# Kernel optimization log

Hardware: AMD Instinct MI355X
Metric: run time of the kernel (lower is better)

Reference implementation:

```python
import jax, jax.numpy as jnp
import numpy as np

DIM = 768
NUM_HEADS = 12
HEAD_DIM = DIM // NUM_HEADS
SCALE = HEAD_DIM ** (-0.5)
LN_EPS = 1e-5


def setup_inputs() -> dict:
    key = jax.random.key(0)
    ks = jax.random.split(key, 8)
    B, K, C = 4, 2048, DIM
    return {
        "x": jax.random.normal(ks[0], (B, K, C), jnp.float32),
        "pos_embed": jax.random.normal(ks[1], (B, K, C), jnp.float32),
        "rel_pos_bias": jax.random.normal(ks[2], (B, K, K), jnp.float32),
        "ln_g": jnp.ones((C,), jnp.float32),
        "ln_b": jnp.zeros((C,), jnp.float32),
        "qkv_w": jax.random.normal(ks[3], (C, 3 * C), jnp.float32) * 0.02,
        "qkv_b": jnp.zeros((3 * C,), jnp.float32),
        "proj_w": jax.random.normal(ks[4], (C, C), jnp.float32) * 0.02,
        "proj_b": jnp.zeros((C,), jnp.float32),
    }


def _layernorm(x, g, b):
    mu = jnp.mean(x, axis=-1, keepdims=True)
    var = jnp.mean(jnp.square(x - mu), axis=-1, keepdims=True)
    return (x - mu) * jax.lax.rsqrt(var + LN_EPS) * g + b


def reference(x, pos_embed, rel_pos_bias, ln_g, ln_b, qkv_w, qkv_b, proj_w, proj_b):
    B, K, C = x.shape
    H, D = NUM_HEADS, HEAD_DIM
    xp = _layernorm(x, ln_g, ln_b) + pos_embed
    qkv = xp @ qkv_w + qkv_b                      # [B,K,3C]
    qkv = qkv.reshape(B, K, 3, H, D)
    q = jnp.transpose(qkv[:, :, 0], (0, 2, 1, 3))  # [B,H,K,D]
    k = jnp.transpose(qkv[:, :, 1], (0, 2, 1, 3))
    v = jnp.transpose(qkv[:, :, 2], (0, 2, 1, 3))
    attn = jnp.einsum("bhqd,bhkd->bhqk", q, k) * SCALE
    attn = attn + rel_pos_bias[:, None, :, :]
    attn = jax.nn.softmax(attn, axis=-1)
    out = jnp.einsum("bhqk,bhkd->bhqd", attn, v)   # [B,H,K,D]
    out = jnp.transpose(out, (0, 2, 1, 3)).reshape(B, K, C)
    # DropPath(0.1) is identity in eval mode
    return out @ proj_w + proj_b
```

## Files before the change

kernel.cpp:

```cpp
#include <hip/hip_runtime.h>
#include <hip/hip_bf16.h>
#include <stdint.h>

typedef __attribute__((ext_vector_type(4))) float f32x4;
typedef __attribute__((ext_vector_type(16))) float f32x16;
typedef __attribute__((ext_vector_type(8))) short s16x8;
typedef __attribute__((ext_vector_type(4))) short s16x4;
typedef uint16_t u16;

#define DEV __device__ __forceinline__

static DEV u16 f2bf(float f) {
  union { float f; uint32_t u; } v; v.f = f;
  uint32_t r = v.u + 0x7fffu + ((v.u >> 16) & 1u);
  return (u16)(r >> 16);
}

static DEV float bf2f(u16 x) {
  union { uint32_t u; float f; } v; v.u = ((uint32_t)x) << 16;
  return v.f;
}

static DEV uint32_t cvt_pk_bf16(float lo, float hi) {
  uint32_t r;
  asm("v_cvt_pk_bf16_f32 %0, %1, %2" : "=v"(r) : "v"(lo), "v"(hi));
  return r;
}

#if defined(__has_builtin) && __has_builtin(__builtin_amdgcn_exp2f)
static DEV float exp2_fast(float x) { return __builtin_amdgcn_exp2f(x); }
#else
static DEV float exp2_fast(float x) {
  float r;
  asm("v_exp_f32 %0, %1\n\ts_nop 1" : "=v"(r) : "v"(x));
  return r;
}
#endif

#define GLD_LDS16(gp, lp) __builtin_amdgcn_global_load_lds( \
    (const __attribute__((address_space(1))) void*)(gp),    \
    (__attribute__((address_space(3))) void*)(lp), 16, 0, 0)

__global__ __launch_bounds__(256) void k_ln(
    const float* __restrict__ x, const float* __restrict__ pos,
    const float* __restrict__ g, const float* __restrict__ be,
    u16* __restrict__ xp) {
  int row = blockIdx.x;
  size_t base = (size_t)row * 768;
  int t = threadIdx.x;
  float v0 = x[base + t], v1 = x[base + t + 256], v2 = x[base + t + 512];
  float s = v0 + v1 + v2;
  float ss = v0 * v0 + v1 * v1 + v2 * v2;
#pragma unroll
  for (int off = 1; off < 64; off <<= 1) {
    s += __shfl_xor(s, off);
    ss += __shfl_xor(ss, off);
  }
  __shared__ float red[8];
  int wave = t >> 6, lane = t & 63;
  if (lane == 0) { red[wave] = s; red[4 + wave] = ss; }
  __syncthreads();
  float tot = red[0] + red[1] + red[2] + red[3];
  float tss = red[4] + red[5] + red[6] + red[7];
  float mu = tot * (1.0f / 768.0f);
  float var = tss * (1.0f / 768.0f) - mu * mu;
  float rs = rsqrtf(var + 1e-5f);
  float vv[3] = {v0, v1, v2};
#pragma unroll
  for (int i = 0; i < 3; ++i) {
    int c = t + i * 256;
    float val = (vv[i] - mu) * rs * g[c] + be[c] + pos[base + c];
    xp[base + c] = f2bf(val);
  }
}

__global__ __launch_bounds__(256) void k_tr(
    const float* __restrict__ in, u16* __restrict__ out, int K, int N) {
  __shared__ float tile[32][33];
  int n0 = blockIdx.x * 32, k0 = blockIdx.y * 32;
  int tx = threadIdx.x & 31, ty = threadIdx.x >> 5;
#pragma unroll
  for (int r = ty; r < 32; r += 8)
    tile[r][tx] = in[(size_t)(k0 + r) * N + n0 + tx];
  __syncthreads();
#pragma unroll
  for (int r = ty; r < 32; r += 8)
    out[(size_t)(n0 + r) * K + k0 + tx] = f2bf(tile[tx][r]);
}

__global__ __launch_bounds__(256) void k_gemm_qkv(
    const u16* __restrict__ A, const u16* __restrict__ Bt,
    const float* __restrict__ bias, u16* __restrict__ qkv,
    u16* __restrict__ vtg, const float* __restrict__ biasf,
    u16* __restrict__ biasb) {
  __shared__ u16 Al[128 * 64];
  __shared__ u16 Bl[128 * 64];
  const size_t BHKD = (size_t)48 * 2048 * 64;
  int mt = blockIdx.x, nt = blockIdx.y;
  int t = threadIdx.x, wave = t >> 6, lane = t & 63;
  int lr = lane & 15, lg = lane >> 4;
  {
    size_t tid = ((size_t)(nt * 64 + mt) * 256 + t) * 8;
    size_t stride = (size_t)1152 * 256 * 8;
    const size_t NB = (size_t)4 * 2048 * 2048;
    for (size_t i = tid; i < NB; i += stride) {
      f32x4 a = *(const f32x4*)(biasf + i);
      f32x4 b = *(const f32x4*)(biasf + i + 4);
      s16x8 o;
#pragma unroll
      for (int j = 0; j < 4; ++j) o[j] = (short)f2bf(a[j] * 1.4426950409f);
#pragma unroll
      for (int j = 0; j < 4; ++j) o[4 + j] = (short)f2bf(b[j] * 1.4426950409f);
      *(s16x8*)(biasb + i) = o;
    }
  }
  f32x4 acc[4][4];
#pragma unroll
  for (int i = 0; i < 4; ++i)
#pragma unroll
    for (int j = 0; j < 4; ++j) acc[i][j] = (f32x4){0.f, 0.f, 0.f, 0.f};
  const size_t Ab = (size_t)mt * 128 * 768;
  const size_t Bb = (size_t)nt * 128 * 768;
  int wr = (wave >> 1) * 64, wc = (wave & 1) * 64;
  for (int kt = 0; kt < 12; ++kt) {
#pragma unroll
    for (int c = 0; c < 4; ++c) {
      int q = c * 256 + t;
      int row = q >> 3, ch = q & 7;
      int sc = ch ^ (row & 7);
      GLD_LDS16(A + Ab + (size_t)row * 768 + kt * 64 + sc * 8,
                &Al[(size_t)(c * 256 + wave * 64) * 8]);
      GLD_LDS16(Bt + Bb + (size_t)row * 768 + kt * 64 + sc * 8,
                &Bl[(size_t)(c * 256 + wave * 64) * 8]);
    }
    __syncthreads();
#pragma unroll
    for (int ki = 0; ki < 2; ++ki) {
      s16x8 af[4], bf[4];
#pragma unroll
      for (int mi = 0; mi < 4; ++mi)
        af[mi] = *(const s16x8*)&Al[(wr + mi * 16 + lr) * 64 +
                                    (((ki * 4 + lg) ^ (lr & 7)) * 8)];
#pragma unroll
      for (int ni = 0; ni < 4; ++ni)
        bf[ni] = *(const s16x8*)&Bl[(wc + ni * 16 + lr) * 64 +
                                    (((ki * 4 + lg) ^ (lr & 7)) * 8)];
#pragma unroll
      for (int mi = 0; mi < 4; ++mi)
#pragma unroll
        for (int ni = 0; ni < 4; ++ni)
          acc[mi][ni] = __builtin_amdgcn_mfma_f32_16x16x32_bf16(
              af[mi], bf[ni], acc[mi][ni], 0, 0, 0);
    }
    __syncthreads();
  }
  int which0 = (nt * 128) / 768;
  float qscale = (which0 == 0) ? 0.1803368801f : 1.0f;
#pragma unroll
  for (int ni = 0; ni < 4; ++ni) {
    int col = wc + ni * 16 + lr;
    int n = nt * 128 + col;
    int which = n / 768, cc = n % 768;
    int h = cc >> 6, d = cc & 63;
    float bs = bias[n];
    if (which == 2) {
#pragma unroll
      for (int mi = 0; mi < 4; ++mi) {
        int m0 = mt * 128 + wr + mi * 16 + lg * 4;
        int b = m0 >> 11, kp0 = m0 & 2047;
        s16x4 o4;
#pragma unroll
        for (int j = 0; j < 4; ++j) o4[j] = (short)f2bf(acc[mi][ni][j] + bs);
        *(s16x4*)&vtg[((size_t)(b * 12 + h) * 64 + d) * 2048 + kp0] = o4;
      }
    } else {
#pragma unroll
      for (int mi = 0; mi < 4; ++mi) {
#pragma unroll
        for (int j = 0; j < 4; ++j) {
          int row = wr + mi * 16 + lg * 4 + j;
          int m = mt * 128 + row;
          int b = m >> 11, kp = m & 2047;
          size_t dst = (size_t)which * BHKD +
                       (((size_t)b * 12 + h) * 2048 + kp) * 64 + d;
          qkv[dst] = f2bf((acc[mi][ni][j] + bs) * qscale);
        }
      }
    }
  }
}

#define STAGE_KV(KB, VB, ktt) do {                                          \
  _Pragma("unroll")                                                         \
  for (int c_ = 0; c_ < 2; ++c_) {                                          \
    int q_ = c_ * 256 + t; int r_ = q_ >> 3, ch_ = q_ & 7;                  \
    int sc_ = ch_ ^ (r_ & 7);                                               \
    int gk_ = (r_ & 0x33) | ((r_ & 4) << 1) | ((r_ & 8) >> 1);              \
    GLD_LDS16(Kg + ((size_t)((ktt) * 64 + gk_)) * 64 + sc_ * 8,             \
              &KB[(c_ * 256 + wave * 64) * 8]);                             \
    GLD_LDS16(Vt + (size_t)r_ * 2048 + (ktt) * 64 + sc_ * 8,                \
              &VB[(c_ * 256 + wave * 64) * 8]);                             \
  }                                                                         \
} while (0)

#define LOAD_B(BR, ktt) do {                                                \
  const u16* bp_ = Bgl + (ktt) * 64;                                        \
  BR[0] = *(const s16x8*)(bp_);                                             \
  BR[1] = *(const s16x8*)(bp_ + 16);                                        \
  BR[2] = *(const s16x8*)(bp_ + 32);                                        \
  BR[3] = *(const s16x8*)(bp_ + 48);                                        \
} while (0)

#define COMPUTE_TILE(KB, VB, BV) do {                                       \
  f32x16 sa_[2];                                                            \
  _Pragma("unroll")                                                         \
  for (int kv_ = 0; kv_ < 2; ++kv_)                                         \
    _Pragma("unroll")                                                       \
    for (int r = 0; r < 16; ++r)                                            \
      sa_[kv_][r] = bf2f((u16)BV[kv_ * 2 + (r >> 3)][r & 7]);               \
  __builtin_amdgcn_s_setprio(1);                                            \
  _Pragma("unroll")                                                         \
  for (int ki = 0; ki < 4; ++ki) {                                          \
    _Pragma("unroll")                                                       \
    for (int kv_ = 0; kv_ < 2; ++kv_) {                                     \
      s16x8 kf = *(const s16x8*)&KB[(kv_ * 32 + l31) * 64 +                 \
                                    (((ki * 2 + hi) ^ (l31 & 7)) * 8)];     \
      sa_[kv_] = __builtin_amdgcn_mfma_f32_32x32x16_bf16(kf, qf[ki],        \
                                                         sa_[kv_], 0, 0, 0);\
    }                                                                       \
  }                                                                         \
  __builtin_amdgcn_s_setprio(0);                                            \
  float p_[32];                                                             \
  _Pragma("unroll")                                                         \
  for (int kv_ = 0; kv_ < 2; ++kv_)                                         \
    _Pragma("unroll")                                                       \
    for (int r = 0; r < 16; ++r)                                            \
      p_[kv_ * 16 + r] = exp2_fast(sa_[kv_][r]);                            \
  float tm_[16];                                                            \
  _Pragma("unroll")                                                         \
  for (int i = 0; i < 16; ++i) tm_[i] = p_[i] + p_[i + 16];                 \
  _Pragma("unroll")                                                         \
  for (int off = 8; off >= 1; off >>= 1)                                    \
    _Pragma("unroll")                                                       \
    for (int i = 0; i < off; ++i) tm_[i] += tm_[i + off];                   \
  l_run += tm_[0];                                                          \
  union { uint32_t u[4]; s16x8 v; } pa_[4];                                 \
  _Pragma("unroll")                                                         \
  for (int s = 0; s < 4; ++s)                                               \
    _Pragma("unroll")                                                       \
    for (int w = 0; w < 4; ++w)                                             \
      pa_[s].u[w] = cvt_pk_bf16(p_[(s >> 1) * 16 + (s & 1) * 8 + 2 * w],    \
                                p_[(s >> 1) * 16 + (s & 1) * 8 + 2 * w + 1]);\
  __builtin_amdgcn_s_setprio(1);                                            \
  _Pragma("unroll")                                                         \
  for (int s = 0; s < 4; ++s) {                                             \
    _Pragma("unroll")                                                       \
    for (int dt = 0; dt < 2; ++dt) {                                        \
      s16x8 vf = *(const s16x8*)&VB[(dt * 32 + l31) * 64 +                  \
                                    (((s * 2 + hi) ^ (l31 & 7)) * 8)];      \
      oacc[dt] = __builtin_amdgcn_mfma_f32_32x32x16_bf16(vf, pa_[s].v,      \
                                                         oacc[dt], 0, 0, 0);\
    }                                                                       \
  }                                                                         \
  __builtin_amdgcn_s_setprio(0);                                            \
} while (0)

__global__ __launch_bounds__(256, 2) void k_attn(
    const u16* __restrict__ qkv, const u16* __restrict__ vtg,
    const u16* __restrict__ biasb, u16* __restrict__ ctx) {
  __shared__ u16 Kl[3][64 * 64];
  __shared__ u16 Vl[3][64 * 64];
  int bid = blockIdx.x;
  int swz = (bid & 7) * 96 + (bid >> 3);
  int h = swz % 12;
  int bq = swz / 12;
  int qt = bq & 15;
  int b = bq >> 4;
  int bh = b * 12 + h;
  int t = threadIdx.x, wave = t >> 6, lane = t & 63;
  int l31 = lane & 31, hi = lane >> 5;
  const size_t BHKD = (size_t)48 * 2048 * 64;
  const u16* Q = qkv + (size_t)bh * 2048 * 64;
  const u16* Kg = Q + BHKD;
  const u16* Vt = vtg + (size_t)bh * 64 * 2048;
  int qrow = qt * 128 + wave * 32 + l31;
  const u16* Bgl = biasb + ((size_t)b * 2048 + qrow) * 2048 + hi * 8;
  s16x8 qf[4];
#pragma unroll
  for (int ki = 0; ki < 4; ++ki)
    qf[ki] = *(const s16x8*)&Q[(size_t)qrow * 64 + ki * 16 + hi * 8];
  f32x16 oacc[2];
#pragma unroll
  for (int r = 0; r < 16; ++r) { oacc[0][r] = 0.f; oacc[1][r] = 0.f; }
  float l_run = 0.f;

  STAGE_KV(Kl[0], Vl[0], 0);
  STAGE_KV(Kl[1], Vl[1], 1);
  asm volatile("s_waitcnt vmcnt(4)" ::: "memory");
  __builtin_amdgcn_s_barrier();
  __builtin_amdgcn_sched_barrier(0);

  int cur = 0;
#pragma unroll 1
  for (int kt = 0; kt < 32; ++kt) {
    s16x8 bv_[4];
    LOAD_B(bv_, kt);
    int nb = cur + 2; if (nb >= 3) nb -= 3;
    if (kt + 2 < 32) STAGE_KV(Kl[nb], Vl[nb], kt + 2);
    COMPUTE_TILE(Kl[cur], Vl[cur], bv_);
    asm volatile("s_waitcnt vmcnt(4)" ::: "memory");
    __builtin_amdgcn_sched_barrier(0);
    __builtin_amdgcn_s_barrier();
    __builtin_amdgcn_sched_barrier(0);
    cur = cur + 1; if (cur >= 3) cur = 0;
  }
  float l_tot = l_run + __shfl_xor(l_run, 32);
  float inv = 1.0f / l_tot;
  size_t obase = ((size_t)b * 2048 + qrow) * 768 + h * 64;
#pragma unroll
  for (int dt = 0; dt < 2; ++dt) {
#pragma unroll
    for (int g = 0; g < 4; ++g) {
      s16x4 o4;
#pragma unroll
      for (int j = 0; j < 4; ++j)
        o4[j] = (short)f2bf(oacc[dt][g * 4 + j] * inv);
      *(s16x4*)&ctx[obase + dt * 32 + g * 8 + hi * 4] = o4;
    }
  }
}

__global__ __launch_bounds__(256) void k_gemm_proj(
    const u16* __restrict__ A, const u16* __restrict__ Bt,
    const float* __restrict__ bias, float* __restrict__ out) {
  __shared__ u16 Al[128 * 64];
  __shared__ u16 Bl[128 * 64];
  int mt = blockIdx.x, nt = blockIdx.y;
  int t = threadIdx.x, wave = t >> 6, lane = t & 63;
  int lr = lane & 15, lg = lane >> 4;
  f32x4 acc[4][4];
#pragma unroll
  for (int i = 0; i < 4; ++i)
#pragma unroll
    for (int j = 0; j < 4; ++j) acc[i][j] = (f32x4){0.f, 0.f, 0.f, 0.f};
  const size_t Ab = (size_t)mt * 128 * 768;
  const size_t Bb = (size_t)nt * 128 * 768;
  int wr = (wave >> 1) * 64, wc = (wave & 1) * 64;
  for (int kt = 0; kt < 12; ++kt) {
#pragma unroll
    for (int c = 0; c < 4; ++c) {
      int q = c * 256 + t;
      int row = q >> 3, ch = q & 7;
      int sc = ch ^ (row & 7);
      GLD_LDS16(A + Ab + (size_t)row * 768 + kt * 64 + sc * 8,
                &Al[(size_t)(c * 256 + wave * 64) * 8]);
      GLD_LDS16(Bt + Bb + (size_t)row * 768 + kt * 64 + sc * 8,
                &Bl[(size_t)(c * 256 + wave * 64) * 8]);
    }
    __syncthreads();
#pragma unroll
    for (int ki = 0; ki < 2; ++ki) {
      s16x8 af[4], bf[4];
#pragma unroll
      for (int mi = 0; mi < 4; ++mi)
        af[mi] = *(const s16x8*)&Al[(wr + mi * 16 + lr) * 64 +
                                    (((ki * 4 + lg) ^ (lr & 7)) * 8)];
#pragma unroll
      for (int ni = 0; ni < 4; ++ni)
        bf[ni] = *(const s16x8*)&Bl[(wc + ni * 16 + lr) * 64 +
                                    (((ki * 4 + lg) ^ (lr & 7)) * 8)];
#pragma unroll
      for (int mi = 0; mi < 4; ++mi)
#pragma unroll
        for (int ni = 0; ni < 4; ++ni)
          acc[mi][ni] = __builtin_amdgcn_mfma_f32_16x16x32_bf16(
              af[mi], bf[ni], acc[mi][ni], 0, 0, 0);
    }
    __syncthreads();
  }
#pragma unroll
  for (int ni = 0; ni < 4; ++ni) {
    int col = wc + ni * 16 + lr;
    int n = nt * 128 + col;
    float bs = bias[n];
#pragma unroll
    for (int mi = 0; mi < 4; ++mi) {
#pragma unroll
      for (int j = 0; j < 4; ++j) {
        int row = wr + mi * 16 + lg * 4 + j;
        out[(size_t)(mt * 128 + row) * 768 + n] = acc[mi][ni][j] + bs;
      }
    }
  }
}

extern "C" void kernel_launch(void* const* d_in, const int* in_sizes, int n_in,
                              void* d_out, int out_size, void* d_ws, size_t ws_size,
                              hipStream_t stream) {
  const float* x      = (const float*)d_in[0];
  const float* pos    = (const float*)d_in[1];
  const float* bias   = (const float*)d_in[2];
  const float* ln_g   = (const float*)d_in[3];
  const float* ln_b   = (const float*)d_in[4];
  const float* qkv_w  = (const float*)d_in[5];
  const float* qkv_b  = (const float*)d_in[6];
  const float* proj_w = (const float*)d_in[7];
  const float* proj_b = (const float*)d_in[8];
  float* out = (float*)d_out;

  char* ws = (char*)d_ws;
  u16* xp      = (u16*)ws;              ws += 12582912;
  u16* qkv_wt  = (u16*)ws;              ws += 3538944;
  u16* proj_wt = (u16*)ws;              ws += 1179648;
  u16* qkvbuf  = (u16*)ws;              ws += 25165824;
  u16* ctx     = (u16*)ws;              ws += 12582912;
  u16* vtg     = (u16*)ws;              ws += 12582912;
  u16* biasb   = (u16*)ws;              ws += 33554432;

  k_ln<<<8192, 256, 0, stream>>>(x, pos, ln_g, ln_b, xp);
  k_tr<<<dim3(72, 24), 256, 0, stream>>>(qkv_w, qkv_wt, 768, 2304);
  k_tr<<<dim3(24, 24), 256, 0, stream>>>(proj_w, proj_wt, 768, 768);
  k_gemm_qkv<<<dim3(64, 18), 256, 0, stream>>>(xp, qkv_wt, qkv_b, qkvbuf, vtg,
                                               bias, biasb);
  k_attn<<<768, 256, 0, stream>>>(qkvbuf, vtg, biasb, ctx);
  k_gemm_proj<<<dim3(64, 6), 256, 0, stream>>>(ctx, proj_wt, proj_b, out);
}
```

Before: 181.2 us.

## Split attention KV range across two blocks and combine partial outputs

```diff
diff --git a/kernel.cpp b/kernel.cpp
--- a/kernel.cpp
+++ b/kernel.cpp
@@ -267,13 +267,16 @@
 
 __global__ __launch_bounds__(256, 2) void k_attn(
     const u16* __restrict__ qkv, const u16* __restrict__ vtg,
-    const u16* __restrict__ biasb, u16* __restrict__ ctx) {
-  __shared__ u16 Kl[3][64 * 64];
-  __shared__ u16 Vl[3][64 * 64];
+    const u16* __restrict__ biasb, u16* __restrict__ ctx,
+    u16* __restrict__ opart1, float* __restrict__ lpart) {
+  __shared__ u16 Kl[2][64 * 64];
+  __shared__ u16 Vl[2][64 * 64];
   int bid = blockIdx.x;
-  int swz = (bid & 7) * 96 + (bid >> 3);
+  int swz = (bid & 7) * 192 + (bid >> 3);
   int h = swz % 12;
-  int bq = swz / 12;
+  int tmp = swz / 12;
+  int half = tmp & 1;
+  int bq = tmp >> 1;
   int qt = bq & 15;
   int b = bq >> 4;
   int bh = b * 12 + h;
@@ -293,29 +296,30 @@
 #pragma unroll
   for (int r = 0; r < 16; ++r) { oacc[0][r] = 0.f; oacc[1][r] = 0.f; }
   float l_run = 0.f;
-
-  STAGE_KV(Kl[0], Vl[0], 0);
-  STAGE_KV(Kl[1], Vl[1], 1);
-  asm volatile("s_waitcnt vmcnt(4)" ::: "memory");
+  int kt0 = half * 16;
+
+  STAGE_KV(Kl[0], Vl[0], kt0);
+  asm volatile("s_waitcnt vmcnt(0)" ::: "memory");
   __builtin_amdgcn_s_barrier();
   __builtin_amdgcn_sched_barrier(0);
 
   int cur = 0;
 #pragma unroll 1
-  for (int kt = 0; kt < 32; ++kt) {
+  for (int kt = 0; kt < 16; ++kt) {
     s16x8 bv_[4];
-    LOAD_B(bv_, kt);
-    int nb = cur + 2; if (nb >= 3) nb -= 3;
-    if (kt + 2 < 32) STAGE_KV(Kl[nb], Vl[nb], kt + 2);
+    LOAD_B(bv_, kt0 + kt);
+    if (kt + 1 < 16) STAGE_KV(Kl[cur ^ 1], Vl[cur ^ 1], kt0 + kt + 1);
     COMPUTE_TILE(Kl[cur], Vl[cur], bv_);
-    asm volatile("s_waitcnt vmcnt(4)" ::: "memory");
+    asm volatile("s_waitcnt vmcnt(0)" ::: "memory");
     __builtin_amdgcn_sched_barrier(0);
     __builtin_amdgcn_s_barrier();
     __builtin_amdgcn_sched_barrier(0);
-    cur = cur + 1; if (cur >= 3) cur = 0;
-  }
-  float l_tot = l_run + __shfl_xor(l_run, 32);
-  float inv = 1.0f / l_tot;
+    cur ^= 1;
+  }
+  float l_half = l_run + __shfl_xor(l_run, 32);
+  int p = (bh * 16 + qt) * 2 + half;
+  if (hi == 0) lpart[p * 128 + wave * 32 + l31] = l_half;
+  u16* op = half ? opart1 : ctx;
   size_t obase = ((size_t)b * 2048 + qrow) * 768 + h * 64;
 #pragma unroll
   for (int dt = 0; dt < 2; ++dt) {
@@ -324,9 +328,31 @@
       s16x4 o4;
 #pragma unroll
       for (int j = 0; j < 4; ++j)
-        o4[j] = (short)f2bf(oacc[dt][g * 4 + j] * inv);
-      *(s16x4*)&ctx[obase + dt * 32 + g * 8 + hi * 4] = o4;
-    }
+        o4[j] = (short)f2bf(oacc[dt][g * 4 + j]);
+      *(s16x4*)&op[obase + dt * 32 + g * 8 + hi * 4] = o4;
+    }
+  }
+}
+
+__global__ __launch_bounds__(256) void k_comb(
+    u16* __restrict__ ctx, const u16* __restrict__ op1,
+    const float* __restrict__ lpart) {
+  int qt = blockIdx.x, bh = blockIdx.y;
+  int b = bh / 12, h = bh - b * 12;
+  int t = threadIdx.x;
+  int q = t >> 1, dh = (t & 1) * 32;
+  int p = (bh * 16 + qt) * 2;
+  float inv = 1.0f / (lpart[p * 128 + q] + lpart[(p + 1) * 128 + q]);
+  size_t base = ((size_t)(b * 2048 + qt * 128 + q)) * 768 + h * 64 + dh;
+#pragma unroll
+  for (int c = 0; c < 4; ++c) {
+    s16x8 a = *(const s16x8*)&ctx[base + c * 8];
+    s16x8 bb = *(const s16x8*)&op1[base + c * 8];
+    s16x8 o;
+#pragma unroll
+    for (int i = 0; i < 8; ++i)
+      o[i] = (short)f2bf((bf2f((u16)a[i]) + bf2f((u16)bb[i])) * inv);
+    *(s16x8*)&ctx[base + c * 8] = o;
   }
 }
 
@@ -416,12 +442,14 @@
   u16* ctx     = (u16*)ws;              ws += 12582912;
   u16* vtg     = (u16*)ws;              ws += 12582912;
   u16* biasb   = (u16*)ws;              ws += 33554432;
+  float* lpart = (float*)ws;            ws += 786432;
 
   k_ln<<<8192, 256, 0, stream>>>(x, pos, ln_g, ln_b, xp);
   k_tr<<<dim3(72, 24), 256, 0, stream>>>(qkv_w, qkv_wt, 768, 2304);
   k_tr<<<dim3(24, 24), 256, 0, stream>>>(proj_w, proj_wt, 768, 768);
   k_gemm_qkv<<<dim3(64, 18), 256, 0, stream>>>(xp, qkv_wt, qkv_b, qkvbuf, vtg,
                                                bias, biasb);
-  k_attn<<<768, 256, 0, stream>>>(qkvbuf, vtg, biasb, ctx);
+  k_attn<<<1536, 256, 0, stream>>>(qkvbuf, vtg, biasb, ctx, xp, lpart);
+  k_comb<<<dim3(16, 48), 256, 0, stream>>>(ctx, xp, lpart);
   k_gemm_proj<<<dim3(64, 6), 256, 0, stream>>>(ctx, proj_wt, proj_b, out);
 }
```

After: 193.9 us. +7.0%, slower.
